# Performance work log

Measured on AMD Instinct MI355X. Metric: run time of the kernel, lower is better.

## Reference

```python
import jax, jax.numpy as jnp
import numpy as np

IMG = 512
LEVELS = (2, 3, 4, 5, 6)
SIZES = (16.0, 32.0, 64.0, 128.0, 256.0)
SCALES = tuple(2.0 ** (i / 3.0) for i in range(3))
ASPECTS = (0.5, 1.0, 2.0)
PRE_NMS = 1000
POST_NMS = 1000
IOU_T = 0.7
SCORE_T = 0.0
CROP = 7
NUM_CLASSES = 80

PARAMS = ('w_l2','b_l2','w_l3','b_l3','w_l4','b_l4','w_l5','b_l5','w_l6','b_l6',
          'w_o2','b_o2','w_o3','b_o3','w_o4','b_o4','w_o5','b_o5','w_o6','b_o6',
          'w_rpn','b_rpn','w_obj','b_obj','w_dlt','b_dlt',
          'w_fc1','b_fc1','w_fc2','b_fc2','w_box','b_box','w_cls','b_cls')

def conv(x, w, b, relu=False):
    y = jax.lax.conv_general_dilated(x, w, (1, 1), 'SAME', dimension_numbers=('NHWC', 'HWIO', 'NHWC')) + b
    return jax.nn.relu(y) if relu else y

def upsample2(x):
    return jnp.repeat(jnp.repeat(x, 2, axis=1), 2, axis=2)

def maxpool2(x):
    return jax.lax.reduce_window(x, -jnp.inf, jax.lax.max, (1, 2, 2, 1), (1, 2, 2, 1), 'VALID')

def make_anchors():
    # keras_cv AnchorGenerator: yxyx, 3 scales x 3 aspect ratios per location, clipped to image
    levels = []
    for lvl, size in zip(LEVELS, SIZES):
        stride = 2 ** lvl
        fs = IMG // stride
        ctr = (np.arange(fs) + 0.5) * stride
        hw = np.array([[size * sc / np.sqrt(ar), size * sc * np.sqrt(ar)] for sc in SCALES for ar in ASPECTS])
        cyx = np.stack(np.meshgrid(ctr, ctr, indexing='ij'), -1)  # [fs,fs,2]
        a = np.concatenate([cyx[:, :, None, :] - hw / 2.0, cyx[:, :, None, :] + hw / 2.0], -1).reshape(-1, 4)
        levels.append(np.clip(a, 0.0, IMG))
    return jnp.asarray(np.concatenate(levels, 0), jnp.float32)  # [196416,4]

def fpn(c2, c3, c4, c5, p):
    c6 = maxpool2(c5)
    p6 = conv(c6, p['w_l6'], p['b_l6'])
    p5 = conv(c5, p['w_l5'], p['b_l5']) + upsample2(p6)
    p4 = conv(c4, p['w_l4'], p['b_l4']) + upsample2(p5)
    p3 = conv(c3, p['w_l3'], p['b_l3']) + upsample2(p4)
    p2 = conv(c2, p['w_l2'], p['b_l2']) + upsample2(p3)
    return [conv(x, p['w_o%d' % l], p['b_o%d' % l]) for x, l in zip((p2, p3, p4, p5, p6), LEVELS)]

def rpn(fmaps, p):
    boxes, scores = [], []
    for f in fmaps:
        t = conv(f, p['w_rpn'], p['b_rpn'], relu=True)
        s = conv(t, p['w_obj'], p['b_obj'])
        d = conv(t, p['w_dlt'], p['b_dlt'])
        B = f.shape[0]
        boxes.append(d.reshape(B, -1, 4))
        scores.append(s.reshape(B, -1))
    return jnp.concatenate(boxes, 1), jnp.concatenate(scores, 1)

def decode(anchors, deltas):
    # _decode_deltas_to_boxes (no variance) then center_yxhw -> yxyx
    ahw = anchors[:, 2:] - anchors[:, :2]
    act = anchors[:, :2] + ahw * 0.5
    cyx = deltas[..., :2] * ahw + act
    hw = jnp.exp(deltas[..., 2:]) * ahw
    return jnp.concatenate([cyx - hw * 0.5, cyx + hw * 0.5], -1)

def nms_single(boxes, scores):
    # greedy NMS on top PRE_NMS proposals, padded to POST_NMS outputs
    sc, order = jax.lax.top_k(scores, PRE_NMS)
    b = boxes[order]
    y1, x1, y2, x2 = b[:, 0], b[:, 1], b[:, 2], b[:, 3]
    area = (y2 - y1) * (x2 - x1)

    def body(i, keep):
        iy1 = jnp.maximum(y1[i], y1)
        ix1 = jnp.maximum(x1[i], x1)
        iy2 = jnp.minimum(y2[i], y2)
        ix2 = jnp.minimum(x2[i], x2)
        inter = jnp.maximum(iy2 - iy1, 0.0) * jnp.maximum(ix2 - ix1, 0.0)
        iou = inter / (area[i] + area - inter + 1e-8)
        suppress = (iou > IOU_T) & (jnp.arange(PRE_NMS) > i) & keep[i]
        return keep & (~suppress)

    keep = jax.lax.fori_loop(0, PRE_NMS, body, sc > SCORE_T)
    idx = jnp.cumsum(keep) - 1
    slot = jnp.where(keep & (idx < POST_NMS), idx, POST_NMS)
    return jnp.zeros((POST_NMS, 4), boxes.dtype).at[slot].set(b, mode='drop')

def pad_stack(fmaps):
    Hm = fmaps[0].shape[1]
    return jnp.stack([jnp.pad(f, ((0, 0), (0, Hm - f.shape[1]), (0, Hm - f.shape[2]), (0, 0))) for f in fmaps], 1)

def roi_align(feats, rois):
    # multilevel crop-and-resize: 14x14 bilinear samples (offset 0.5) -> 2x2 avg pool -> 7x7
    S = CROP * 2

    def one(feat, box):
        h = box[2] - box[0]
        w = box[3] - box[1]
        size = jnp.sqrt(jnp.maximum(h * w, 1e-8))
        lvl = jnp.clip(jnp.floor(jnp.log2(size / 224.0) + 4.0), 2, 6).astype(jnp.int32)
        stride_i = jnp.left_shift(1, lvl)
        stride = stride_i.astype(jnp.float32)
        fs_i = IMG // stride_i
        fs = fs_i.astype(jnp.float32)
        yy = jnp.clip(box[0] / stride + (jnp.arange(S) + 0.5) * (h / stride) / S - 0.5, 0.0, fs - 1.0)
        xx = jnp.clip(box[1] / stride + (jnp.arange(S) + 0.5) * (w / stride) / S - 0.5, 0.0, fs - 1.0)
        y0 = jnp.floor(yy).astype(jnp.int32)
        x0 = jnp.floor(xx).astype(jnp.int32)
        y1 = jnp.minimum(y0 + 1, fs_i - 1)
        x1 = jnp.minimum(x0 + 1, fs_i - 1)
        wy = (yy - y0)[:, None, None]
        wx = (xx - x0)[None, :, None]
        fm = feat[lvl - 2]
        v00 = fm[y0[:, None], x0[None, :]]
        v01 = fm[y0[:, None], x1[None, :]]
        v10 = fm[y1[:, None], x0[None, :]]
        v11 = fm[y1[:, None], x1[None, :]]
        val = (1.0 - wy) * ((1.0 - wx) * v00 + wx * v01) + wy * ((1.0 - wx) * v10 + wx * v11)
        return val.reshape(CROP, 2, CROP, 2, val.shape[-1]).mean(axis=(1, 3))

    return jax.vmap(lambda f, r: jax.vmap(lambda b: one(f, b))(r))(feats, rois)

def forward(c2, c3, c4, c5, p):
    fmaps = fpn(c2, c3, c4, c5, p)
    rpn_boxes, rpn_scores = rpn(fmaps, p)
    anchors = make_anchors()
    decoded = decode(anchors, rpn_boxes)
    rois = jax.lax.stop_gradient(jax.vmap(nms_single)(decoded, rpn_scores))  # [B,1000,4]
    feats = roi_align(pad_stack(fmaps), rois)  # [B,1000,7,7,256]
    B, R = feats.shape[0], feats.shape[1]
    x = feats.reshape(B, R, -1)
    x = jax.nn.relu(x @ p['w_fc1'] + p['b_fc1'])
    x = jax.nn.relu(x @ p['w_fc2'] + p['b_fc2'])
    return rois, x @ p['w_box'] + p['b_box'], x @ p['w_cls'] + p['b_cls']

def setup_inputs() -> dict:
    key = jax.random.key(0)
    ks = iter(jax.random.split(key, 64))
    def rnd(shape, s=1.0):
        return jax.random.normal(next(ks), shape, jnp.float32) * s
    B = 2
    inp = {
        'c2': rnd((B, 128, 128, 256)), 'c3': rnd((B, 64, 64, 512)),
        'c4': rnd((B, 32, 32, 1024)), 'c5': rnd((B, 16, 16, 2048)),
    }
    lat_in = {2: 256, 3: 512, 4: 1024, 5: 2048, 6: 2048}
    for l in LEVELS:
        inp['w_l%d' % l] = rnd((1, 1, lat_in[l], 256), 0.02)
        inp['b_l%d' % l] = jnp.zeros((256,), jnp.float32)
        inp['w_o%d' % l] = rnd((3, 3, 256, 256), 0.02)
        inp['b_o%d' % l] = jnp.zeros((256,), jnp.float32)
    inp['w_rpn'] = rnd((3, 3, 256, 256), 0.02); inp['b_rpn'] = jnp.zeros((256,), jnp.float32)
    inp['w_obj'] = rnd((1, 1, 256, 9), 0.02); inp['b_obj'] = jnp.zeros((9,), jnp.float32)
    inp['w_dlt'] = rnd((1, 1, 256, 36), 0.02); inp['b_dlt'] = jnp.zeros((36,), jnp.float32)
    F = CROP * CROP * 256
    inp['w_fc1'] = rnd((F, 1024), 0.01); inp['b_fc1'] = jnp.zeros((1024,), jnp.float32)
    inp['w_fc2'] = rnd((1024, 1024), 0.02); inp['b_fc2'] = jnp.zeros((1024,), jnp.float32)
    inp['w_box'] = rnd((1024, 4), 0.02); inp['b_box'] = jnp.zeros((4,), jnp.float32)
    inp['w_cls'] = rnd((1024, NUM_CLASSES + 1), 0.02); inp['b_cls'] = jnp.zeros((NUM_CLASSES + 1,), jnp.float32)
    return inp

def reference(c2, c3, c4, c5, w_l2, b_l2, w_l3, b_l3, w_l4, b_l4, w_l5, b_l5, w_l6, b_l6,
              w_o2, b_o2, w_o3, b_o3, w_o4, b_o4, w_o5, b_o5, w_o6, b_o6,
              w_rpn, b_rpn, w_obj, b_obj, w_dlt, b_dlt,
              w_fc1, b_fc1, w_fc2, b_fc2, w_box, b_box, w_cls, b_cls):
    loc = locals()
    p = {k: loc[k] for k in PARAMS}
    return forward(c2, c3, c4, c5, p)
```

## Files before the change

### kernel.cpp

```cpp
#include <hip/hip_runtime.h>
#include <math.h>


#define NUM_ANCH 196416

typedef double d4 __attribute__((ext_vector_type(4)));
typedef __attribute__((ext_vector_type(8))) short bf8_t;
typedef __attribute__((ext_vector_type(4))) float f4_t;
typedef _Float16 h8_t __attribute__((ext_vector_type(8)));

__device__ inline unsigned short f2bf(float x) {
  unsigned u = __float_as_uint(x);
  unsigned r = (u + 0x7fffu + ((u >> 16) & 1u)) >> 16;
  return (unsigned short)r;
}
__device__ inline float bf2f(unsigned short h) {
  return __uint_as_float(((unsigned)h) << 16);
}

__global__ void maxpool_kernel(const float* __restrict__ in, float* __restrict__ out) {
  int idx = blockIdx.x * 256 + threadIdx.x;
  int c = idx & 2047;
  int x = (idx >> 11) & 7;
  int y = (idx >> 14) & 7;
  int b = idx >> 17;
  const float* p = in + (((size_t)b * 16 + 2 * y) * 16 + 2 * x) * 2048 + c;
  float m = fmaxf(fmaxf(p[0], p[2048]), fmaxf(p[16 * 2048], p[16 * 2048 + 2048]));
  out[idx] = m;
}

template <int CIN>
__global__ __launch_bounds__(256) void lateral_d(
    const float* __restrict__ in, const float* __restrict__ w,
    const float* __restrict__ bias, double* __restrict__ out) {
  const int t = threadIdx.x;
  const size_t pix0 = (size_t)blockIdx.x * 4;
  double b = (double)bias[t];
  double a0 = b, a1 = b, a2 = b, a3 = b;
  const float* i0 = in + pix0 * CIN;
  for (int ci = 0; ci < CIN; ++ci) {
    double wv = (double)w[ci * 256 + t];
    a0 += (double)i0[ci] * wv;
    a1 += (double)i0[CIN + ci] * wv;
    a2 += (double)i0[2 * CIN + ci] * wv;
    a3 += (double)i0[3 * CIN + ci] * wv;
  }
  out[(pix0 + 0) * 256 + t] = a0;
  out[(pix0 + 1) * 256 + t] = a1;
  out[(pix0 + 2) * 256 + t] = a2;
  out[(pix0 + 3) * 256 + t] = a3;
}

__global__ void upadd_d(double* __restrict__ fine, const double* __restrict__ coarse,
                        int Hf, int Wf) {
  int idx = blockIdx.x * 256 + threadIdx.x;
  int c = idx & 255;
  int rem = idx >> 8;
  int x = rem % Wf; rem /= Wf;
  int y = rem % Hf;
  int b = rem / Hf;
  fine[idx] += coarse[(((size_t)b * (Hf >> 1) + (y >> 1)) * (Wf >> 1) + (x >> 1)) * 256 + c];
}

__global__ __launch_bounds__(256) void wsplit_f16(
    const float* __restrict__ W, unsigned short* __restrict__ PH,
    unsigned short* __restrict__ PL) {
  int id = blockIdx.x * 256 + threadIdx.x;
  int co = id & 255, ci = (id >> 8) & 255, p9 = id >> 16;
  float w = W[id];
  _Float16 wh = (_Float16)w;
  float rw = (w - (float)wh) * 4096.0f;
  _Float16 wl = (_Float16)rw;
  int q = (p9 * 8 + (ci >> 5)) * 16 + (co >> 4);
  int idx = q * 512 + (co & 15) * 32 + (ci & 31);
  PH[idx] = __builtin_bit_cast(unsigned short, wh);
  PL[idx] = __builtin_bit_cast(unsigned short, wl);
}

struct ConvArgsH {
  const double* in[5];
  double* out[5];
  const unsigned short* wH[5];
  const unsigned short* wL[5];
  const float* bias[5];
  int H[5];
  int nbx[5];
  int off[6];
};

template <bool RELU>
__global__ __launch_bounds__(256) void conv3x3_h2(ConvArgsH A) {
  __shared__ uint4 smemq[34816 / 16];
  char* sh = (char*)smemq;
  const int bx = blockIdx.x;
  int l = 0;
#pragma unroll
  for (int i = 1; i < 5; ++i)
    if (bx >= A.off[i]) l = i;
  const int rel = bx - A.off[l];
  const int H = A.H[l];
  const int W = H;
  const int nbx = A.nbx[l];
  const int x0 = (rel % nbx) * 32;
  const int y = (rel / nbx) % H;
  const int b = rel / (nbx * H);
  const double* __restrict__ in = A.in[l];
  double* __restrict__ out = A.out[l];
  const unsigned short* __restrict__ wHp = A.wH[l];
  const unsigned short* __restrict__ wLp = A.wL[l];
  const float* __restrict__ bias = A.bias[l];

  const int t = threadIdx.x;
  const int lane = t & 63;
  const int wq = t >> 6;
  const int lm = lane & 15;
  const int lq = lane >> 4;

  d4 dacc[2][4];
#pragma unroll
  for (int mt = 0; mt < 2; ++mt)
#pragma unroll
    for (int nt = 0; nt < 4; ++nt) {
      double bv = (double)bias[wq * 64 + nt * 16 + lm];
      dacc[mt][nt] = (d4){bv, bv, bv, bv};
    }

  const int cst = (t & 127) * 2;
  const int prow = t >> 7;

  for (int ky = 0; ky < 3; ++ky) {
    const int gy = y + ky - 1;
    __syncthreads();
    for (int pp = prow; pp < 34; pp += 2) {
      int gx = x0 + pp - 1;
      double xv0 = 0.0, xv1 = 0.0;
      if (gy >= 0 && gy < H && gx >= 0 && gx < W) {
        const double* ptr = in + (((size_t)b * H + gy) * W + gx) * 256 + cst;
        xv0 = ptr[0];
        xv1 = ptr[1];
      }
      _Float16 h0 = (_Float16)((float)xv0);
      _Float16 h1 = (_Float16)((float)xv1);
      float r0 = (float)(xv0 - (double)(float)h0) * 4096.0f;
      float r1 = (float)(xv1 - (double)(float)h1) * 4096.0f;
      _Float16 l0 = (_Float16)r0, l1 = (_Float16)r1;
      unsigned hp = (unsigned)__builtin_bit_cast(unsigned short, h0) |
                    ((unsigned)__builtin_bit_cast(unsigned short, h1) << 16);
      unsigned lp = (unsigned)__builtin_bit_cast(unsigned short, l0) |
                    ((unsigned)__builtin_bit_cast(unsigned short, l1) << 16);
      int bo = pp * 512 + ((cst * 2) ^ ((pp & 7) << 4));
      *(unsigned*)(sh + bo) = hp;
      *(unsigned*)(sh + 17408 + bo) = lp;
    }
    __syncthreads();

    f4_t accA[2][4], accB[2][4];
#pragma unroll
    for (int mt = 0; mt < 2; ++mt)
#pragma unroll
      for (int nt = 0; nt < 4; ++nt) {
        accA[mt][nt] = (f4_t){0.f, 0.f, 0.f, 0.f};
        accB[mt][nt] = (f4_t){0.f, 0.f, 0.f, 0.f};
      }

    for (int kx = 0; kx < 3; ++kx) {
      const int P0 = (ky * 3 + kx) * 8;
      for (int kt = 0; kt < 8; ++kt) {
        h8_t aH[2], aL[2];
#pragma unroll
        for (int mt = 0; mt < 2; ++mt) {
          int pix = mt * 16 + lm + kx;
          int bo = pix * 512 + ((kt * 64 + lq * 16) ^ ((pix & 7) << 4));
          aH[mt] = *(const h8_t*)(sh + bo);
          aL[mt] = *(const h8_t*)(sh + 17408 + bo);
        }
        h8_t bH[4], bL[4];
#pragma unroll
        for (int nt = 0; nt < 4; ++nt) {
          size_t eo = (size_t)((P0 + kt) * 16 + wq * 4 + nt) * 512 + lm * 32 + lq * 8;
          bH[nt] = *(const h8_t*)(wHp + eo);
          bL[nt] = *(const h8_t*)(wLp + eo);
        }
#pragma unroll
        for (int mt = 0; mt < 2; ++mt)
#pragma unroll
          for (int nt = 0; nt < 4; ++nt) {
            accB[mt][nt] = __builtin_amdgcn_mfma_f32_16x16x32_f16(aH[mt], bL[nt], accB[mt][nt], 0, 0, 0);
            accB[mt][nt] = __builtin_amdgcn_mfma_f32_16x16x32_f16(aL[mt], bH[nt], accB[mt][nt], 0, 0, 0);
            accA[mt][nt] = __builtin_amdgcn_mfma_f32_16x16x32_f16(aH[mt], bH[nt], accA[mt][nt], 0, 0, 0);
          }
      }
    }
#pragma unroll
    for (int mt = 0; mt < 2; ++mt)
#pragma unroll
      for (int nt = 0; nt < 4; ++nt)
#pragma unroll
        for (int r = 0; r < 4; ++r)
          dacc[mt][nt][r] += (double)accA[mt][nt][r] +
                             (double)accB[mt][nt][r] * (1.0 / 4096.0);
  }

#pragma unroll
  for (int mt = 0; mt < 2; ++mt)
#pragma unroll
    for (int nt = 0; nt < 4; ++nt) {
      int cout = wq * 64 + nt * 16 + lm;
#pragma unroll
      for (int r = 0; r < 4; ++r) {
        int gx = x0 + mt * 16 + lq * 4 + r;
        if (gx < W) {
          double v = dacc[mt][nt][r];
          if (RELU) v = fmax(v, 0.0);
          out[(((size_t)b * H + y) * W + gx) * 256 + cout] = v;
        }
      }
    }
}

struct AnchorHW { double hh[9]; double ww[9]; };

__global__ __launch_bounds__(64) void rpn_head_d(
    const double* __restrict__ tmap,
    const float* __restrict__ w_obj, const float* __restrict__ b_obj,
    const float* __restrict__ w_dlt, const float* __restrict__ b_dlt,
    double* __restrict__ scores, double* __restrict__ boxes,
    int H, int W, int a_off, double stride, AnchorHW anc) {
  __shared__ double tv[256];
  __shared__ double dlt[36];
  const int t = threadIdx.x;
  const int x = blockIdx.x, y = blockIdx.y, b = blockIdx.z;
  const double* px = tmap + (((size_t)b * H + y) * W + x) * 256;
  tv[t] = px[t]; tv[t + 64] = px[t + 64]; tv[t + 128] = px[t + 128]; tv[t + 192] = px[t + 192];
  __syncthreads();
  double sacc = 0.0;
  if (t < 9) {
    sacc = (double)b_obj[t];
    for (int ci = 0; ci < 256; ++ci) sacc += tv[ci] * (double)w_obj[ci * 9 + t];
  } else if (t < 45) {
    int j = t - 9;
    double a = (double)b_dlt[j];
    for (int ci = 0; ci < 256; ++ci) a += tv[ci] * (double)w_dlt[ci * 36 + j];
    dlt[j] = a;
  }
  __syncthreads();
  if (t < 9) {
    int ai = a_off + (y * W + x) * 9 + t;
    scores[(size_t)b * NUM_ANCH + ai] = sacc;
    double cy = (y + 0.5) * stride, cx = (x + 0.5) * stride;
    double hh = anc.hh[t], ww = anc.ww[t];
    float ay1 = (float)fmin(fmax(cy - hh * 0.5, 0.0), 512.0);
    float ax1 = (float)fmin(fmax(cx - ww * 0.5, 0.0), 512.0);
    float ay2 = (float)fmin(fmax(cy + hh * 0.5, 0.0), 512.0);
    float ax2 = (float)fmin(fmax(cx + ww * 0.5, 0.0), 512.0);
    float ahf = ay2 - ay1, awf = ax2 - ax1;
    float actyf = ay1 + ahf * 0.5f, actxf = ax1 + awf * 0.5f;
    double dy = dlt[t * 4 + 0], dx = dlt[t * 4 + 1];
    double dh = dlt[t * 4 + 2], dw = dlt[t * 4 + 3];
    double ncy = dy * (double)ahf + (double)actyf;
    double ncx = dx * (double)awf + (double)actxf;
    double nh = exp(dh) * (double)ahf;
    double nw = exp(dw) * (double)awf;
    double* bo = boxes + ((size_t)b * NUM_ANCH + ai) * 4;
    bo[0] = ncy - nh * 0.5;
    bo[1] = ncx - nw * 0.5;
    bo[2] = ncy + nh * 0.5;
    bo[3] = ncx + nw * 0.5;
  }
}

__device__ inline unsigned long long dkey(double f) {
  unsigned long long u = (unsigned long long)__double_as_longlong(f);
  return u ^ ((unsigned long long)((long long)u >> 63) | 0x8000000000000000ull);
}

__global__ __launch_bounds__(1024) void topk_d(
    const double* __restrict__ scores, const double* __restrict__ boxes,
    double* __restrict__ ss, double* __restrict__ sb) {
  const int A = NUM_ANCH;
  __shared__ unsigned hist[256];
  __shared__ unsigned long long kk[2048];
  __shared__ unsigned id[2048];
  __shared__ unsigned long long s_prefix;
  __shared__ unsigned s_need, s_cnt;
  const int b = blockIdx.x, t = threadIdx.x;
  const double* sc = scores + (size_t)b * A;
  if (t == 0) { s_prefix = 0ull; s_need = 1000; s_cnt = 0; }
  __syncthreads();
  for (int r = 0; r < 8; ++r) {
    if (t < 256) hist[t] = 0;
    __syncthreads();
    const int shift = 56 - 8 * r;
    const unsigned long long prefix = s_prefix;
    unsigned long long maskHigh = 0ull;
    if (r != 0) maskHigh = (~0ull) << (shift + 8);
    for (int i = t; i < A; i += 1024) {
      unsigned long long k = dkey(sc[i]);
      if ((k & maskHigh) == prefix) atomicAdd(&hist[(unsigned)(k >> shift) & 255u], 1u);
    }
    __syncthreads();
    if (t == 0) {
      unsigned need = s_need, cum = 0;
      for (int bin = 255; bin >= 0; --bin) {
        cum += hist[bin];
        if (cum >= need) {
          s_prefix = prefix | ((unsigned long long)bin << shift);
          s_need = need - (cum - hist[bin]);
          break;
        }
      }
    }
    __syncthreads();
  }
  const unsigned long long K = s_prefix;
  for (int i = t; i < A; i += 1024) {
    unsigned long long k = dkey(sc[i]);
    if (k >= K) {
      unsigned pos = atomicAdd(&s_cnt, 1u);
      if (pos < 2048) { kk[pos] = k; id[pos] = (unsigned)i; }
    }
  }
  __syncthreads();
  unsigned cnt = s_cnt;
  for (int i = t; i < 2048; i += 1024)
    if (i >= cnt) { kk[i] = 0ull; id[i] = 0xFFFFFFFFu; }
  __syncthreads();
  for (int k = 2; k <= 2048; k <<= 1) {
    for (int j = k >> 1; j > 0; j >>= 1) {
#pragma unroll
      for (int u = 0; u < 2; ++u) {
        int i = t + u * 1024;
        int ixj = i ^ j;
        if (ixj > i) {
          unsigned long long ka = kk[i], kc = kk[ixj];
          unsigned ia = id[i], ic = id[ixj];
          bool cPrec = (kc > ka) || (kc == ka && ic < ia);
          bool up = (i & k) != 0;
          if (cPrec != up) { kk[i] = kc; kk[ixj] = ka; id[i] = ic; id[ixj] = ia; }
        }
      }
      __syncthreads();
    }
  }
  if (t < 1000) {
    unsigned idx = id[t];
    ss[b * 1000 + t] = sc[idx];
    const double* bp = boxes + ((size_t)b * A + idx) * 4;
    double* op = sb + (b * 1000 + t) * 4;
    op[0] = bp[0]; op[1] = bp[1]; op[2] = bp[2]; op[3] = bp[3];
  }
}

__global__ void suppmat_d(const double* __restrict__ sb,
                          unsigned long long* __restrict__ supp) {
  int g = blockIdx.x * 256 + threadIdx.x;
  int w = g & 15;
  int i = (g >> 4) % 1000;
  int b = g / 16000;
  const double* bx = sb + b * 4000;
  double y1 = bx[i * 4 + 0], x1 = bx[i * 4 + 1], y2 = bx[i * 4 + 2], x2 = bx[i * 4 + 3];
  double ai = (y2 - y1) * (x2 - x1);
  unsigned long long m = 0;
  for (int q = 0; q < 64; ++q) {
    int j = w * 64 + q;
    if (j > i && j < 1000) {
      double by1 = bx[j * 4 + 0], bx1 = bx[j * 4 + 1], by2 = bx[j * 4 + 2], bx2 = bx[j * 4 + 3];
      double aj = (by2 - by1) * (bx2 - bx1);
      double iy1 = fmax(y1, by1), ix1 = fmax(x1, bx1);
      double iy2 = fmin(y2, by2), ix2 = fmin(x2, bx2);
      double inter = fmax(iy2 - iy1, 0.0) * fmax(ix2 - ix1, 0.0);
      double iou = inter / (ai + aj - inter + 1e-8);
      if (iou > 0.7) m |= (1ull << q);
    }
  }
  supp[g] = m;
}

__global__ __launch_bounds__(64) void nms_reduce_d(
    const double* __restrict__ ss, const double* __restrict__ sb,
    const unsigned long long* __restrict__ supp,
    float* __restrict__ rois, double* __restrict__ rois64) {
  __shared__ unsigned long long aliveS[16];
  __shared__ int pref[16];
  const int b = blockIdx.x, lane = threadIdx.x;
  unsigned long long myword = 0;
  if (lane < 16) {
    for (int q = 0; q < 64; ++q) {
      int j = lane * 64 + q;
      if (j < 1000 && ss[b * 1000 + j] > 0.0) myword |= (1ull << q);
    }
  }
  const unsigned long long* sp = supp + (size_t)b * 16000;
  unsigned long long cur = (lane < 16) ? sp[lane] : 0ull;
  for (int i = 0; i < 1000; ++i) {
    unsigned long long nxt = (lane < 16 && i < 999) ? sp[(i + 1) * 16 + lane] : 0ull;
    unsigned long long wv = __shfl(myword, i >> 6);
    if ((wv >> (i & 63)) & 1ull) {
      if (lane < 16) myword &= ~cur;
    }
    cur = nxt;
  }
  if (lane < 16) aliveS[lane] = myword;
  __syncthreads();
  if (lane == 0) {
    int s = 0;
    for (int w = 0; w < 16; ++w) { pref[w] = s; s += __popcll(aliveS[w]); }
  }
  float* ro = rois + b * 4000;
  double* rd = rois64 + b * 4000;
  for (int k = lane; k < 4000; k += 64) { ro[k] = 0.0f; rd[k] = 0.0; }
  __syncthreads();
  for (int j = lane; j < 1000; j += 64) {
    int w = j >> 6;
    unsigned long long word = aliveS[w];
    if ((word >> (j & 63)) & 1ull) {
      unsigned long long below = (j & 63) ? (word & ((1ull << (j & 63)) - 1ull)) : 0ull;
      int slot = pref[w] + __popcll(below);
      const double* bp = sb + (b * 1000 + j) * 4;
      ro[slot * 4 + 0] = (float)bp[0]; ro[slot * 4 + 1] = (float)bp[1];
      ro[slot * 4 + 2] = (float)bp[2]; ro[slot * 4 + 3] = (float)bp[3];
      rd[slot * 4 + 0] = bp[0]; rd[slot * 4 + 1] = bp[1];
      rd[slot * 4 + 2] = bp[2]; rd[slot * 4 + 3] = bp[3];
    }
  }
}

__global__ __launch_bounds__(256) void roi_align_d(
    const double* __restrict__ o2, const double* __restrict__ o3,
    const double* __restrict__ o4, const double* __restrict__ o5,
    const double* __restrict__ o6, const double* __restrict__ rois64,
    unsigned short* __restrict__ featsH, unsigned short* __restrict__ featsL) {
  __shared__ double s_wy[14], s_wx[14];
  __shared__ int s_y0[14], s_y1[14], s_x0[14], s_x1[14];
  const int t = threadIdx.x;
  const int b = blockIdx.x / 1000, r = blockIdx.x % 1000;
  const double* box = rois64 + (b * 1000 + r) * 4;
  double b0 = box[0], b1 = box[1], b2 = box[2], b3 = box[3];
  double h = b2 - b0, w = b3 - b1;
  double size = sqrt(fmax(h * w, 1e-8));
  double lf = floor(log2(size / 224.0) + 4.0);
  lf = fmin(fmax(lf, 2.0), 6.0);
  int lvl = (int)lf;
  int stride_i = 1 << lvl;
  double stride = (double)stride_i;
  int fs_i = 512 >> lvl;
  double fs = (double)fs_i;
  if (t < 14) {
    double v = b0 / stride + ((t + 0.5) * (h / stride)) / 14.0 - 0.5;
    v = fmin(fmax(v, 0.0), fs - 1.0);
    int i0 = (int)floor(v);
    s_y0[t] = i0; s_y1[t] = min(i0 + 1, fs_i - 1); s_wy[t] = v - (double)i0;
  } else if (t >= 64 && t < 78) {
    int u = t - 64;
    double v = b1 / stride + ((u + 0.5) * (w / stride)) / 14.0 - 0.5;
    v = fmin(fmax(v, 0.0), fs - 1.0);
    int i0 = (int)floor(v);
    s_x0[u] = i0; s_x1[u] = min(i0 + 1, fs_i - 1); s_wx[u] = v - (double)i0;
  }
  __syncthreads();
  const double* omaps[5] = {o2, o3, o4, o5, o6};
  const double* fm = omaps[lvl - 2] + (size_t)b * fs_i * fs_i * 256 + t;
  size_t obase = ((size_t)(b * 1000 + r) * 49) * 256 + t;
  for (int oy = 0; oy < 7; ++oy) {
    double acc[7] = {0, 0, 0, 0, 0, 0, 0};
#pragma unroll
    for (int sy = 0; sy < 2; ++sy) {
      int yy = oy * 2 + sy;
      int y0 = s_y0[yy], y1 = s_y1[yy];
      double wy = s_wy[yy];
      const double* r0 = fm + (size_t)y0 * fs_i * 256;
      const double* r1 = fm + (size_t)y1 * fs_i * 256;
      for (int ox = 0; ox < 7; ++ox) {
#pragma unroll
        for (int sx = 0; sx < 2; ++sx) {
          int xx = ox * 2 + sx;
          int x0 = s_x0[xx], x1 = s_x1[xx];
          double wx = s_wx[xx];
          double v00 = r0[x0 * 256], v01 = r0[x1 * 256];
          double v10 = r1[x0 * 256], v11 = r1[x1 * 256];
          double val = (1.0 - wy) * ((1.0 - wx) * v00 + wx * v01) +
                       wy * ((1.0 - wx) * v10 + wx * v11);
          acc[ox] += val;
        }
      }
    }
    for (int ox = 0; ox < 7; ++ox) {
      float v = (float)(acc[ox] * 0.25);
      unsigned short hh = f2bf(v);
      size_t idx = obase + (size_t)(oy * 7 + ox) * 256;
      featsH[idx] = hh;
      featsL[idx] = f2bf(v - bf2f(hh));
    }
  }
}

__global__ __launch_bounds__(256) void split_transpose(
    const float* __restrict__ W, unsigned short* __restrict__ TH,
    unsigned short* __restrict__ TL, int K, int N) {
  __shared__ unsigned short shh[32 * 33], shl[32 * 33];
  const int kt = blockIdx.y * 32, nt = blockIdx.x * 32;
  const int tx = threadIdx.x & 31, ty = threadIdx.x >> 5;
  for (int yy = ty; yy < 32; yy += 8) {
    float v = W[(size_t)(kt + yy) * N + nt + tx];
    unsigned short h = f2bf(v);
    shh[yy * 33 + tx] = h;
    shl[yy * 33 + tx] = f2bf(v - bf2f(h));
  }
  __syncthreads();
  for (int yy = ty; yy < 32; yy += 8) {
    TH[(size_t)(nt + yy) * K + kt + tx] = shh[tx * 33 + yy];
    TL[(size_t)(nt + yy) * K + kt + tx] = shl[tx * 33 + yy];
  }
}

struct GemmPArgs {
  const unsigned short* AH;
  const unsigned short* AL;
  const unsigned short* BTH;
  const unsigned short* BTL;
  float* P[4];
  int M, N, K, KC;
};

__global__ __launch_bounds__(256) void gemm_mfma_partial(GemmPArgs G) {
  __shared__ __align__(16) unsigned short AsH[128 * 40], AsL[128 * 40];
  __shared__ __align__(16) unsigned short BsH[128 * 40], BsL[128 * 40];
  const int t = threadIdx.x;
  const int lane = t & 63;
  const int wave = t >> 6;
  const int lm = lane & 15, lq = lane >> 4;
  const int wn = wave & 1, wm = wave >> 1;
  const int m0 = blockIdx.y * 128, n0 = blockIdx.x * 128;
  const int kc = blockIdx.z;
  const int kbeg = kc * G.KC, kend = kbeg + G.KC;
  const int M = G.M, N = G.N, K = G.K;
  float* __restrict__ C = G.P[kc];
  const unsigned short* __restrict__ AH = G.AH;
  const unsigned short* __restrict__ AL = G.AL;
  const unsigned short* __restrict__ BTH = G.BTH;
  const unsigned short* __restrict__ BTL = G.BTL;
  const int sr = t >> 1;
  const int sk = (t & 1) * 16;

  f4_t acc[4][4];
#pragma unroll
  for (int mt = 0; mt < 4; ++mt)
#pragma unroll
    for (int nt = 0; nt < 4; ++nt) acc[mt][nt] = (f4_t){0.f, 0.f, 0.f, 0.f};

  const uint4 zz = {0u, 0u, 0u, 0u};
  for (int k0 = kbeg; k0 < kend; k0 += 32) {
    __syncthreads();
    {
      uint4 vh0 = zz, vh1 = zz, vl0 = zz, vl1 = zz;
      if (m0 + sr < M) {
        size_t off = (size_t)(m0 + sr) * K + k0 + sk;
        vh0 = *(const uint4*)&AH[off];
        vh1 = *(const uint4*)&AH[off + 8];
        vl0 = *(const uint4*)&AL[off];
        vl1 = *(const uint4*)&AL[off + 8];
      }
      *(uint4*)&AsH[sr * 40 + sk] = vh0;
      *(uint4*)&AsH[sr * 40 + sk + 8] = vh1;
      *(uint4*)&AsL[sr * 40 + sk] = vl0;
      *(uint4*)&AsL[sr * 40 + sk + 8] = vl1;
    }
    {
      size_t off = (size_t)(n0 + sr) * K + k0 + sk;
      *(uint4*)&BsH[sr * 40 + sk] = *(const uint4*)&BTH[off];
      *(uint4*)&BsH[sr * 40 + sk + 8] = *(const uint4*)&BTH[off + 8];
      *(uint4*)&BsL[sr * 40 + sk] = *(const uint4*)&BTL[off];
      *(uint4*)&BsL[sr * 40 + sk + 8] = *(const uint4*)&BTL[off + 8];
    }
    __syncthreads();

    bf8_t aH[4], aL[4], bH[4], bL[4];
#pragma unroll
    for (int mt = 0; mt < 4; ++mt) {
      int idx = (wm * 64 + mt * 16 + lm) * 40 + lq * 8;
      aH[mt] = *(const bf8_t*)&AsH[idx];
      aL[mt] = *(const bf8_t*)&AsL[idx];
    }
#pragma unroll
    for (int nt = 0; nt < 4; ++nt) {
      int idx = (wn * 64 + nt * 16 + lm) * 40 + lq * 8;
      bH[nt] = *(const bf8_t*)&BsH[idx];
      bL[nt] = *(const bf8_t*)&BsL[idx];
    }
#pragma unroll
    for (int mt = 0; mt < 4; ++mt)
#pragma unroll
      for (int nt = 0; nt < 4; ++nt) {
        f4_t a0 = acc[mt][nt];
        a0 = __builtin_amdgcn_mfma_f32_16x16x32_bf16(aL[mt], bH[nt], a0, 0, 0, 0);
        a0 = __builtin_amdgcn_mfma_f32_16x16x32_bf16(aH[mt], bL[nt], a0, 0, 0, 0);
        a0 = __builtin_amdgcn_mfma_f32_16x16x32_bf16(aH[mt], bH[nt], a0, 0, 0, 0);
        acc[mt][nt] = a0;
      }
  }
#pragma unroll
  for (int mt = 0; mt < 4; ++mt) {
#pragma unroll
    for (int nt = 0; nt < 4; ++nt) {
      int ncol = n0 + wn * 64 + nt * 16 + lm;
#pragma unroll
      for (int r = 0; r < 4; ++r) {
        int m = m0 + wm * 64 + mt * 16 + lq * 4 + r;
        if (m < M) C[(size_t)m * N + ncol] = acc[mt][nt][r];
      }
    }
  }
}

__global__ void reduce4_split(const float* __restrict__ p0, const float* __restrict__ p1,
                              const float* __restrict__ p2, const float* __restrict__ p3,
                              const float* __restrict__ bias,
                              unsigned short* __restrict__ H, unsigned short* __restrict__ L,
                              int n) {
  int i = blockIdx.x * 256 + threadIdx.x;
  if (i < n) {
    float v = ((p0[i] + p1[i]) + p2[i]) + p3[i] + bias[i & 1023];
    v = fmaxf(v, 0.0f);
    unsigned short h = f2bf(v);
    H[i] = h;
    L[i] = f2bf(v - bf2f(h));
  }
}

__global__ void reduce4_f32(const float* __restrict__ p0, const float* __restrict__ p1,
                            const float* __restrict__ p2, const float* __restrict__ p3,
                            const float* __restrict__ bias, float* __restrict__ C, int n) {
  int i = blockIdx.x * 256 + threadIdx.x;
  if (i < n) {
    float v = ((p0[i] + p1[i]) + p2[i]) + p3[i] + bias[i & 1023];
    C[i] = fmaxf(v, 0.0f);
  }
}

__global__ __launch_bounds__(128) void boxcls_kernel(
    const float* __restrict__ x, const float* __restrict__ w_box,
    const float* __restrict__ b_box, const float* __restrict__ w_cls,
    const float* __restrict__ b_cls, float* __restrict__ out) {
  __shared__ float xv[1024];
  const int t = threadIdx.x;
  const int row = blockIdx.x;
  const float* xp = x + (size_t)row * 1024;
#pragma unroll
  for (int k = 0; k < 8; ++k) xv[k * 128 + t] = xp[k * 128 + t];
  __syncthreads();
  if (t < 4) {
    float acc = b_box[t];
    for (int k = 0; k < 1024; ++k) acc += xv[k] * w_box[k * 4 + t];
    out[8000 + row * 4 + t] = acc;
  } else if (t < 85) {
    int j = t - 4;
    float acc = b_cls[j];
    for (int k = 0; k < 1024; ++k) acc += xv[k] * w_cls[k * 81 + j];
    out[16000 + row * 81 + j] = acc;
  }
}

extern "C" void kernel_launch(void* const* d_in, const int* in_sizes, int n_in,
                              void* d_out, int out_size, void* d_ws, size_t ws_size,
                              hipStream_t stream) {
  (void)in_sizes; (void)n_in; (void)out_size; (void)ws_size;

  const float* c_in[4] = {(const float*)d_in[0], (const float*)d_in[1],
                          (const float*)d_in[2], (const float*)d_in[3]};
  const float *w_l[5], *b_l[5], *w_o[5], *b_o[5];
  for (int l = 0; l < 5; ++l) {
    w_l[l] = (const float*)d_in[4 + l * 4 + 0];
    b_l[l] = (const float*)d_in[4 + l * 4 + 1];
    w_o[l] = (const float*)d_in[4 + l * 4 + 2];
    b_o[l] = (const float*)d_in[4 + l * 4 + 3];
  }
  const float* w_rpn = (const float*)d_in[24];
  const float* b_rpn = (const float*)d_in[25];
  const float* w_obj = (const float*)d_in[26];
  const float* b_obj = (const float*)d_in[27];
  const float* w_dlt = (const float*)d_in[28];
  const float* b_dlt = (const float*)d_in[29];
  const float* w_fc1 = (const float*)d_in[30];
  const float* b_fc1 = (const float*)d_in[31];
  const float* w_fc2 = (const float*)d_in[32];
  const float* b_fc2 = (const float*)d_in[33];
  const float* w_box = (const float*)d_in[34];
  const float* b_box = (const float*)d_in[35];
  const float* w_cls = (const float*)d_in[36];
  const float* b_cls = (const float*)d_in[37];

  char* W8 = (char*)d_ws;
  double* o64 = (double*)(W8 + 0);
  double* p64 = (double*)(W8 + 89391104);
  float* c6buf = (float*)(W8 + 178782208);
  double* scores = (double*)(W8 + 179830784);
  double* boxes = (double*)(W8 + 182973440);
  double* ssb = (double*)(W8 + 195544064);
  double* sbb = (double*)(W8 + 195560064);
  double* rois64 = (double*)(W8 + 195624064);
  unsigned long long* suppb = (unsigned long long*)(W8 + 195688064);
  unsigned short* featsH = (unsigned short*)(W8 + 89391104);
  unsigned short* featsL = (unsigned short*)(W8 + 139567104);
  float* fc1b = (float*)(W8 + 0);
  float* fc2b = (float*)(W8 + 8192000);
  unsigned short* wT1H = (unsigned short*)(W8 + 16384000);
  unsigned short* wT1L = (unsigned short*)(W8 + 42074112);
  unsigned short* wT2H = (unsigned short*)(W8 + 67764224);
  unsigned short* wT2L = (unsigned short*)(W8 + 69861376);
  unsigned short* fc1H = (unsigned short*)(W8 + 89391104);
  unsigned short* fc1L = (unsigned short*)(W8 + 93487104);
  float* fc1p1 = (float*)(W8 + 8192000);
  float* fc1p2 = (float*)(W8 + 71958528);
  float* fc1p3 = (float*)(W8 + 80150528);
  float* fc2p1 = (float*)(W8 + 0);
  float* fc2p2 = (float*)(W8 + 16384000);
  float* fc2p3 = (float*)(W8 + 24576000);
  float* outf = (float*)d_out;

  unsigned short* woH[5];
  unsigned short* woL[5];
  for (int l = 0; l < 5; ++l) {
    woH[l] = (unsigned short*)(W8 + 182973440 + (size_t)l * 2359296);
    woL[l] = (unsigned short*)(W8 + 182973440 + (size_t)l * 2359296 + 1179648);
  }
  unsigned short* wrH = (unsigned short*)(W8 + 179830784);
  unsigned short* wrL = (unsigned short*)(W8 + 179830784 + 1179648);

  const size_t OFF[5] = {0, 8388608, 10485760, 11010048, 11141120};
  double* o[5]; double* p[5];
  for (int l = 0; l < 5; ++l) { o[l] = o64 + OFF[l]; p[l] = p64 + OFF[l]; }

  const int HS[5] = {128, 64, 32, 16, 8};
  const int a_off[5] = {0, 147456, 184320, 193536, 195840};
  const double strides[5] = {4.0, 8.0, 16.0, 32.0, 64.0};
  const double SZ[5] = {16.0, 32.0, 64.0, 128.0, 256.0};
  AnchorHW anc[5];
  for (int l = 0; l < 5; ++l) {
    const double ars[3] = {0.5, 1.0, 2.0};
    for (int s = 0; s < 3; ++s) {
      double sc = pow(2.0, s / 3.0);
      for (int a = 0; a < 3; ++a) {
        double sq = sqrt(ars[a]);
        anc[l].hh[s * 3 + a] = SZ[l] * sc / sq;
        anc[l].ww[s * 3 + a] = SZ[l] * sc * sq;
      }
    }
  }

  for (int l = 0; l < 5; ++l)
    wsplit_f16<<<2304, 256, 0, stream>>>(w_o[l], woH[l], woL[l]);
  wsplit_f16<<<2304, 256, 0, stream>>>(w_rpn, wrH, wrL);

  maxpool_kernel<<<1024, 256, 0, stream>>>(c_in[3], c6buf);
  lateral_d<2048><<<32, 256, 0, stream>>>(c6buf, w_l[4], b_l[4], p[4]);
  lateral_d<2048><<<128, 256, 0, stream>>>(c_in[3], w_l[3], b_l[3], p[3]);
  upadd_d<<<512, 256, 0, stream>>>(p[3], p[4], 16, 16);
  lateral_d<1024><<<512, 256, 0, stream>>>(c_in[2], w_l[2], b_l[2], p[2]);
  upadd_d<<<2048, 256, 0, stream>>>(p[2], p[3], 32, 32);
  lateral_d<512><<<2048, 256, 0, stream>>>(c_in[1], w_l[1], b_l[1], p[1]);
  upadd_d<<<8192, 256, 0, stream>>>(p[1], p[2], 64, 64);
  lateral_d<256><<<8192, 256, 0, stream>>>(c_in[0], w_l[0], b_l[0], p[0]);
  upadd_d<<<32768, 256, 0, stream>>>(p[0], p[1], 128, 128);

  ConvArgsH co, ct;
  int total = 0;
  for (int l = 0; l < 5; ++l) {
    int nbx = (HS[l] + 31) / 32;
    co.in[l] = p[l]; co.out[l] = o[l];
    co.wH[l] = woH[l]; co.wL[l] = woL[l]; co.bias[l] = b_o[l];
    ct.in[l] = o[l]; ct.out[l] = p[l];
    ct.wH[l] = wrH;  ct.wL[l] = wrL;  ct.bias[l] = b_rpn;
    co.H[l] = ct.H[l] = HS[l];
    co.nbx[l] = ct.nbx[l] = nbx;
    co.off[l] = ct.off[l] = total;
    total += nbx * HS[l] * 2;
  }
  co.off[5] = ct.off[5] = total;
  conv3x3_h2<false><<<total, 256, 0, stream>>>(co);
  conv3x3_h2<true><<<total, 256, 0, stream>>>(ct);

  for (int l = 0; l < 5; ++l) {
    dim3 g(HS[l], HS[l], 2);
    rpn_head_d<<<g, 64, 0, stream>>>(p[l], w_obj, b_obj, w_dlt, b_dlt, scores, boxes,
                                     HS[l], HS[l], a_off[l], strides[l], anc[l]);
  }
  topk_d<<<2, 1024, 0, stream>>>(scores, boxes, ssb, sbb);
  suppmat_d<<<125, 256, 0, stream>>>(sbb, suppb);
  nms_reduce_d<<<2, 64, 0, stream>>>(ssb, sbb, suppb, outf, rois64);
  roi_align_d<<<2000, 256, 0, stream>>>(o[0], o[1], o[2], o[3], o[4], rois64,
                                        featsH, featsL);
  split_transpose<<<dim3(32, 392), 256, 0, stream>>>(w_fc1, wT1H, wT1L, 12544, 1024);
  split_transpose<<<dim3(32, 32), 256, 0, stream>>>(w_fc2, wT2H, wT2L, 1024, 1024);

  GemmPArgs g1;
  g1.AH = featsH; g1.AL = featsL; g1.BTH = wT1H; g1.BTL = wT1L;
  g1.P[0] = fc1b; g1.P[1] = fc1p1; g1.P[2] = fc1p2; g1.P[3] = fc1p3;
  g1.M = 2000; g1.N = 1024; g1.K = 12544; g1.KC = 3136;
  gemm_mfma_partial<<<dim3(8, 16, 4), 256, 0, stream>>>(g1);
  reduce4_split<<<8000, 256, 0, stream>>>(fc1b, fc1p1, fc1p2, fc1p3, b_fc1,
                                          fc1H, fc1L, 2048000);

  GemmPArgs g2;
  g2.AH = fc1H; g2.AL = fc1L; g2.BTH = wT2H; g2.BTL = wT2L;
  g2.P[0] = fc2b; g2.P[1] = fc2p1; g2.P[2] = fc2p2; g2.P[3] = fc2p3;
  g2.M = 2000; g2.N = 1024; g2.K = 1024; g2.KC = 256;
  gemm_mfma_partial<<<dim3(8, 16, 4), 256, 0, stream>>>(g2);
  reduce4_f32<<<8000, 256, 0, stream>>>(fc2b, fc2p1, fc2p2, fc2p3, b_fc2,
                                        fc2b, 2048000);

  boxcls_kernel<<<2000, 128, 0, stream>>>(fc2b, w_box, b_box, w_cls, b_cls, outf);
}
```

Measured before the change: 3.304 ms.

## Emit pre-split fp16 planes from FPN conv and widen conv blocks to 512 threads

The output conv now writes its result as fp32 (for ROI align) and as pre-split fp16 hi/lo planes, so the RPN conv loads ready fp16 halves with 16-byte vector loads instead of reading doubles and splitting them per tile. The conv block grows to 512 threads (8 waves, each covering 32 output channels instead of 64), which reduces per-wave accumulator registers and uses a launch bound of 4 blocks per CU. ROI align reads fp32 feature maps instead of doubles. The trade-off is reduced precision in the stored output features (fp32, and hi/lo fp16 with a truncated residual) and three separate output writes per element.

```diff
diff --git a/kernel.cpp b/kernel.cpp
--- a/kernel.cpp
+++ b/kernel.cpp
@@ -77,9 +77,14 @@
   PL[idx] = __builtin_bit_cast(unsigned short, wl);
 }
 
-struct ConvArgsH {
-  const double* in[5];
-  double* out[5];
+struct ConvArgsU {
+  const double* inD[5];
+  const unsigned short* inH[5];
+  const unsigned short* inL[5];
+  float* outF[5];
+  unsigned short* outH[5];
+  unsigned short* outL[5];
+  double* outD[5];
   const unsigned short* wH[5];
   const unsigned short* wL[5];
   const float* bias[5];
@@ -88,8 +93,8 @@
   int off[6];
 };
 
-template <bool RELU>
-__global__ __launch_bounds__(256) void conv3x3_h2(ConvArgsH A) {
+template <bool PLANES, bool RELU, bool OSPLIT>
+__global__ __launch_bounds__(512, 4) void conv3x3_u(ConvArgsU A) {
   __shared__ uint4 smemq[34816 / 16];
   char* sh = (char*)smemq;
   const int bx = blockIdx.x;
@@ -104,8 +109,6 @@
   const int x0 = (rel % nbx) * 32;
   const int y = (rel / nbx) % H;
   const int b = rel / (nbx * H);
-  const double* __restrict__ in = A.in[l];
-  double* __restrict__ out = A.out[l];
   const unsigned short* __restrict__ wHp = A.wH[l];
   const unsigned short* __restrict__ wLp = A.wL[l];
   const float* __restrict__ bias = A.bias[l];
@@ -116,49 +119,70 @@
   const int lm = lane & 15;
   const int lq = lane >> 4;
 
-  d4 dacc[2][4];
+  d4 dacc[2][2];
 #pragma unroll
   for (int mt = 0; mt < 2; ++mt)
 #pragma unroll
-    for (int nt = 0; nt < 4; ++nt) {
-      double bv = (double)bias[wq * 64 + nt * 16 + lm];
+    for (int nt = 0; nt < 2; ++nt) {
+      double bv = (double)bias[wq * 32 + nt * 16 + lm];
       dacc[mt][nt] = (d4){bv, bv, bv, bv};
     }
 
   const int cst = (t & 127) * 2;
   const int prow = t >> 7;
+  const int c16 = (t & 31) * 8;
+  const int pp0 = t >> 5;
 
   for (int ky = 0; ky < 3; ++ky) {
     const int gy = y + ky - 1;
+    const bool rowok = (gy >= 0 && gy < H);
     __syncthreads();
-    for (int pp = prow; pp < 34; pp += 2) {
-      int gx = x0 + pp - 1;
-      double xv0 = 0.0, xv1 = 0.0;
-      if (gy >= 0 && gy < H && gx >= 0 && gx < W) {
-        const double* ptr = in + (((size_t)b * H + gy) * W + gx) * 256 + cst;
-        xv0 = ptr[0];
-        xv1 = ptr[1];
-      }
-      _Float16 h0 = (_Float16)((float)xv0);
-      _Float16 h1 = (_Float16)((float)xv1);
-      float r0 = (float)(xv0 - (double)(float)h0) * 4096.0f;
-      float r1 = (float)(xv1 - (double)(float)h1) * 4096.0f;
-      _Float16 l0 = (_Float16)r0, l1 = (_Float16)r1;
-      unsigned hp = (unsigned)__builtin_bit_cast(unsigned short, h0) |
-                    ((unsigned)__builtin_bit_cast(unsigned short, h1) << 16);
-      unsigned lp = (unsigned)__builtin_bit_cast(unsigned short, l0) |
-                    ((unsigned)__builtin_bit_cast(unsigned short, l1) << 16);
-      int bo = pp * 512 + ((cst * 2) ^ ((pp & 7) << 4));
-      *(unsigned*)(sh + bo) = hp;
-      *(unsigned*)(sh + 17408 + bo) = lp;
+    if (PLANES) {
+      const unsigned short* __restrict__ inH = A.inH[l];
+      const unsigned short* __restrict__ inL = A.inL[l];
+      for (int pp = pp0; pp < 34; pp += 16) {
+        int gx = x0 + pp - 1;
+        uint4 vh = {0u, 0u, 0u, 0u}, vl = {0u, 0u, 0u, 0u};
+        if (rowok && gx >= 0 && gx < W) {
+          size_t base = (((size_t)b * H + gy) * W + gx) * 256 + c16;
+          vh = *(const uint4*)&inH[base];
+          vl = *(const uint4*)&inL[base];
+        }
+        int bo = pp * 512 + ((c16 * 2) ^ ((pp & 7) << 4));
+        *(uint4*)(sh + bo) = vh;
+        *(uint4*)(sh + 17408 + bo) = vl;
+      }
+    } else {
+      const double* __restrict__ inD = A.inD[l];
+      for (int pp = prow; pp < 34; pp += 4) {
+        int gx = x0 + pp - 1;
+        double xv0 = 0.0, xv1 = 0.0;
+        if (rowok && gx >= 0 && gx < W) {
+          const double* ptr = inD + (((size_t)b * H + gy) * W + gx) * 256 + cst;
+          xv0 = ptr[0];
+          xv1 = ptr[1];
+        }
+        _Float16 h0 = (_Float16)((float)xv0);
+        _Float16 h1 = (_Float16)((float)xv1);
+        float r0 = (float)(xv0 - (double)(float)h0) * 4096.0f;
+        float r1 = (float)(xv1 - (double)(float)h1) * 4096.0f;
+        _Float16 l0 = (_Float16)r0, l1 = (_Float16)r1;
+        unsigned hp = (unsigned)__builtin_bit_cast(unsigned short, h0) |
+                      ((unsigned)__builtin_bit_cast(unsigned short, h1) << 16);
+        unsigned lp = (unsigned)__builtin_bit_cast(unsigned short, l0) |
+                      ((unsigned)__builtin_bit_cast(unsigned short, l1) << 16);
+        int bo = pp * 512 + ((cst * 2) ^ ((pp & 7) << 4));
+        *(unsigned*)(sh + bo) = hp;
+        *(unsigned*)(sh + 17408 + bo) = lp;
+      }
     }
     __syncthreads();
 
-    f4_t accA[2][4], accB[2][4];
+    f4_t accA[2][2], accB[2][2];
 #pragma unroll
     for (int mt = 0; mt < 2; ++mt)
 #pragma unroll
-      for (int nt = 0; nt < 4; ++nt) {
+      for (int nt = 0; nt < 2; ++nt) {
         accA[mt][nt] = (f4_t){0.f, 0.f, 0.f, 0.f};
         accB[mt][nt] = (f4_t){0.f, 0.f, 0.f, 0.f};
       }
@@ -174,27 +198,24 @@
           aH[mt] = *(const h8_t*)(sh + bo);
           aL[mt] = *(const h8_t*)(sh + 17408 + bo);
         }
-        h8_t bH[4], bL[4];
-#pragma unroll
-        for (int nt = 0; nt < 4; ++nt) {
-          size_t eo = (size_t)((P0 + kt) * 16 + wq * 4 + nt) * 512 + lm * 32 + lq * 8;
-          bH[nt] = *(const h8_t*)(wHp + eo);
-          bL[nt] = *(const h8_t*)(wLp + eo);
+#pragma unroll
+        for (int nt = 0; nt < 2; ++nt) {
+          size_t eo = (size_t)((P0 + kt) * 16 + wq * 2 + nt) * 512 + lm * 32 + lq * 8;
+          h8_t bH = *(const h8_t*)(wHp + eo);
+          h8_t bL = *(const h8_t*)(wLp + eo);
+#pragma unroll
+          for (int mt = 0; mt < 2; ++mt) {
+            accB[mt][nt] = __builtin_amdgcn_mfma_f32_16x16x32_f16(aH[mt], bL, accB[mt][nt], 0, 0, 0);
+            accB[mt][nt] = __builtin_amdgcn_mfma_f32_16x16x32_f16(aL[mt], bH, accB[mt][nt], 0, 0, 0);
+            accA[mt][nt] = __builtin_amdgcn_mfma_f32_16x16x32_f16(aH[mt], bH, accA[mt][nt], 0, 0, 0);
+          }
         }
-#pragma unroll
-        for (int mt = 0; mt < 2; ++mt)
-#pragma unroll
-          for (int nt = 0; nt < 4; ++nt) {
-            accB[mt][nt] = __builtin_amdgcn_mfma_f32_16x16x32_f16(aH[mt], bL[nt], accB[mt][nt], 0, 0, 0);
-            accB[mt][nt] = __builtin_amdgcn_mfma_f32_16x16x32_f16(aL[mt], bH[nt], accB[mt][nt], 0, 0, 0);
-            accA[mt][nt] = __builtin_amdgcn_mfma_f32_16x16x32_f16(aH[mt], bH[nt], accA[mt][nt], 0, 0, 0);
-          }
       }
     }
 #pragma unroll
     for (int mt = 0; mt < 2; ++mt)
 #pragma unroll
-      for (int nt = 0; nt < 4; ++nt)
+      for (int nt = 0; nt < 2; ++nt)
 #pragma unroll
         for (int r = 0; r < 4; ++r)
           dacc[mt][nt][r] += (double)accA[mt][nt][r] +
@@ -204,15 +225,25 @@
 #pragma unroll
   for (int mt = 0; mt < 2; ++mt)
 #pragma unroll
-    for (int nt = 0; nt < 4; ++nt) {
-      int cout = wq * 64 + nt * 16 + lm;
+    for (int nt = 0; nt < 2; ++nt) {
+      int cout = wq * 32 + nt * 16 + lm;
 #pragma unroll
       for (int r = 0; r < 4; ++r) {
         int gx = x0 + mt * 16 + lq * 4 + r;
         if (gx < W) {
           double v = dacc[mt][nt][r];
           if (RELU) v = fmax(v, 0.0);
-          out[(((size_t)b * H + y) * W + gx) * 256 + cout] = v;
+          size_t idx = (((size_t)b * H + y) * W + gx) * 256 + cout;
+          if (OSPLIT) {
+            _Float16 hh = (_Float16)((float)v);
+            float rr = (float)(v - (double)(float)hh) * 4096.0f;
+            _Float16 ll = (_Float16)rr;
+            A.outF[l][idx] = (float)v;
+            A.outH[l][idx] = __builtin_bit_cast(unsigned short, hh);
+            A.outL[l][idx] = __builtin_bit_cast(unsigned short, ll);
+          } else {
+            A.outD[l][idx] = v;
+          }
         }
       }
     }
@@ -426,9 +457,9 @@
 }
 
 __global__ __launch_bounds__(256) void roi_align_d(
-    const double* __restrict__ o2, const double* __restrict__ o3,
-    const double* __restrict__ o4, const double* __restrict__ o5,
-    const double* __restrict__ o6, const double* __restrict__ rois64,
+    const float* __restrict__ o2, const float* __restrict__ o3,
+    const float* __restrict__ o4, const float* __restrict__ o5,
+    const float* __restrict__ o6, const double* __restrict__ rois64,
     unsigned short* __restrict__ featsH, unsigned short* __restrict__ featsL) {
   __shared__ double s_wy[14], s_wx[14];
   __shared__ int s_y0[14], s_y1[14], s_x0[14], s_x1[14];
@@ -458,8 +489,8 @@
     s_x0[u] = i0; s_x1[u] = min(i0 + 1, fs_i - 1); s_wx[u] = v - (double)i0;
   }
   __syncthreads();
-  const double* omaps[5] = {o2, o3, o4, o5, o6};
-  const double* fm = omaps[lvl - 2] + (size_t)b * fs_i * fs_i * 256 + t;
+  const float* omaps[5] = {o2, o3, o4, o5, o6};
+  const float* fm = omaps[lvl - 2] + (size_t)b * fs_i * fs_i * 256 + t;
   size_t obase = ((size_t)(b * 1000 + r) * 49) * 256 + t;
   for (int oy = 0; oy < 7; ++oy) {
     double acc[7] = {0, 0, 0, 0, 0, 0, 0};
@@ -468,16 +499,16 @@
       int yy = oy * 2 + sy;
       int y0 = s_y0[yy], y1 = s_y1[yy];
       double wy = s_wy[yy];
-      const double* r0 = fm + (size_t)y0 * fs_i * 256;
-      const double* r1 = fm + (size_t)y1 * fs_i * 256;
+      const float* r0 = fm + (size_t)y0 * fs_i * 256;
+      const float* r1 = fm + (size_t)y1 * fs_i * 256;
       for (int ox = 0; ox < 7; ++ox) {
 #pragma unroll
         for (int sx = 0; sx < 2; ++sx) {
           int xx = ox * 2 + sx;
           int x0 = s_x0[xx], x1 = s_x1[xx];
           double wx = s_wx[xx];
-          double v00 = r0[x0 * 256], v01 = r0[x1 * 256];
-          double v10 = r1[x0 * 256], v11 = r1[x1 * 256];
+          double v00 = (double)r0[x0 * 256], v01 = (double)r0[x1 * 256];
+          double v10 = (double)r1[x0 * 256], v11 = (double)r1[x1 * 256];
           double val = (1.0 - wy) * ((1.0 - wx) * v00 + wx * v01) +
                        wy * ((1.0 - wx) * v10 + wx * v11);
           acc[ox] += val;
@@ -690,7 +721,9 @@
   const float* b_cls = (const float*)d_in[37];
 
   char* W8 = (char*)d_ws;
-  double* o64 = (double*)(W8 + 0);
+  float* oF32 = (float*)(W8 + 0);
+  unsigned short* oH = (unsigned short*)(W8 + 44695552);
+  unsigned short* oL = (unsigned short*)(W8 + 67043328);
   double* p64 = (double*)(W8 + 89391104);
   float* c6buf = (float*)(W8 + 178782208);
   double* scores = (double*)(W8 + 179830784);
@@ -727,9 +760,6 @@
   unsigned short* wrL = (unsigned short*)(W8 + 179830784 + 1179648);
 
   const size_t OFF[5] = {0, 8388608, 10485760, 11010048, 11141120};
-  double* o[5]; double* p[5];
-  for (int l = 0; l < 5; ++l) { o[l] = o64 + OFF[l]; p[l] = p64 + OFF[l]; }
-
   const int HS[5] = {128, 64, 32, 16, 8};
   const int a_off[5] = {0, 147456, 184320, 193536, 195840};
   const double strides[5] = {4.0, 8.0, 16.0, 32.0, 64.0};
@@ -752,23 +782,27 @@
   wsplit_f16<<<2304, 256, 0, stream>>>(w_rpn, wrH, wrL);
 
   maxpool_kernel<<<1024, 256, 0, stream>>>(c_in[3], c6buf);
-  lateral_d<2048><<<32, 256, 0, stream>>>(c6buf, w_l[4], b_l[4], p[4]);
-  lateral_d<2048><<<128, 256, 0, stream>>>(c_in[3], w_l[3], b_l[3], p[3]);
-  upadd_d<<<512, 256, 0, stream>>>(p[3], p[4], 16, 16);
-  lateral_d<1024><<<512, 256, 0, stream>>>(c_in[2], w_l[2], b_l[2], p[2]);
-  upadd_d<<<2048, 256, 0, stream>>>(p[2], p[3], 32, 32);
-  lateral_d<512><<<2048, 256, 0, stream>>>(c_in[1], w_l[1], b_l[1], p[1]);
-  upadd_d<<<8192, 256, 0, stream>>>(p[1], p[2], 64, 64);
-  lateral_d<256><<<8192, 256, 0, stream>>>(c_in[0], w_l[0], b_l[0], p[0]);
-  upadd_d<<<32768, 256, 0, stream>>>(p[0], p[1], 128, 128);
-
-  ConvArgsH co, ct;
+  lateral_d<2048><<<32, 256, 0, stream>>>(c6buf, w_l[4], b_l[4], p64 + OFF[4]);
+  lateral_d<2048><<<128, 256, 0, stream>>>(c_in[3], w_l[3], b_l[3], p64 + OFF[3]);
+  upadd_d<<<512, 256, 0, stream>>>(p64 + OFF[3], p64 + OFF[4], 16, 16);
+  lateral_d<1024><<<512, 256, 0, stream>>>(c_in[2], w_l[2], b_l[2], p64 + OFF[2]);
+  upadd_d<<<2048, 256, 0, stream>>>(p64 + OFF[2], p64 + OFF[3], 32, 32);
+  lateral_d<512><<<2048, 256, 0, stream>>>(c_in[1], w_l[1], b_l[1], p64 + OFF[1]);
+  upadd_d<<<8192, 256, 0, stream>>>(p64 + OFF[1], p64 + OFF[2], 64, 64);
+  lateral_d<256><<<8192, 256, 0, stream>>>(c_in[0], w_l[0], b_l[0], p64 + OFF[0]);
+  upadd_d<<<32768, 256, 0, stream>>>(p64 + OFF[0], p64 + OFF[1], 128, 128);
+
+  ConvArgsU co, ct;
   int total = 0;
   for (int l = 0; l < 5; ++l) {
     int nbx = (HS[l] + 31) / 32;
-    co.in[l] = p[l]; co.out[l] = o[l];
+    co.inD[l] = p64 + OFF[l]; co.inH[l] = nullptr; co.inL[l] = nullptr;
+    co.outF[l] = oF32 + OFF[l]; co.outH[l] = oH + OFF[l]; co.outL[l] = oL + OFF[l];
+    co.outD[l] = nullptr;
     co.wH[l] = woH[l]; co.wL[l] = woL[l]; co.bias[l] = b_o[l];
-    ct.in[l] = o[l]; ct.out[l] = p[l];
+    ct.inD[l] = nullptr; ct.inH[l] = oH + OFF[l]; ct.inL[l] = oL + OFF[l];
+    ct.outF[l] = nullptr; ct.outH[l] = nullptr; ct.outL[l] = nullptr;
+    ct.outD[l] = p64 + OFF[l];
     ct.wH[l] = wrH;  ct.wL[l] = wrL;  ct.bias[l] = b_rpn;
     co.H[l] = ct.H[l] = HS[l];
     co.nbx[l] = ct.nbx[l] = nbx;
@@ -776,18 +810,20 @@
     total += nbx * HS[l] * 2;
   }
   co.off[5] = ct.off[5] = total;
-  conv3x3_h2<false><<<total, 256, 0, stream>>>(co);
-  conv3x3_h2<true><<<total, 256, 0, stream>>>(ct);
+  conv3x3_u<false, false, true><<<total, 512, 0, stream>>>(co);
+  conv3x3_u<true, true, false><<<total, 512, 0, stream>>>(ct);
 
   for (int l = 0; l < 5; ++l) {
     dim3 g(HS[l], HS[l], 2);
-    rpn_head_d<<<g, 64, 0, stream>>>(p[l], w_obj, b_obj, w_dlt, b_dlt, scores, boxes,
-                                     HS[l], HS[l], a_off[l], strides[l], anc[l]);
+    rpn_head_d<<<g, 64, 0, stream>>>(p64 + OFF[l], w_obj, b_obj, w_dlt, b_dlt,
+                                     scores, boxes, HS[l], HS[l], a_off[l],
+                                     strides[l], anc[l]);
   }
   topk_d<<<2, 1024, 0, stream>>>(scores, boxes, ssb, sbb);
   suppmat_d<<<125, 256, 0, stream>>>(sbb, suppb);
   nms_reduce_d<<<2, 64, 0, stream>>>(ssb, sbb, suppb, outf, rois64);
-  roi_align_d<<<2000, 256, 0, stream>>>(o[0], o[1], o[2], o[3], o[4], rois64,
+  roi_align_d<<<2000, 256, 0, stream>>>(oF32 + OFF[0], oF32 + OFF[1], oF32 + OFF[2],
+                                        oF32 + OFF[3], oF32 + OFF[4], rois64,
                                         featsH, featsL);
   split_transpose<<<dim3(32, 392), 256, 0, stream>>>(w_fc1, wT1H, wT1L, 12544, 1024);
   split_transpose<<<dim3(32, 32), 256, 0, stream>>>(w_fc2, wT2H, wT2L, 1024, 1024);
```

Result: faster. 3.096 ms (-6.3%).
